# Optimization experiments

Hardware: AMD Instinct MI355X
Metric: run time of the kernel (lower is better)

The kernel has to match this reference:

```python
import jax, jax.numpy as jnp
import numpy as np

B, N, H = 32768, 64, 256
OFF = N * (N - 1) // 2  # 2016


def _xavier(k, shape):
    fan_in, fan_out = shape
    lim = (6.0 / (fan_in + fan_out)) ** 0.5
    return jax.random.uniform(k, shape, jnp.float32, -lim, lim)


def setup_inputs() -> dict:
    key = jax.random.key(0)
    ks = jax.random.split(key, 8)
    return {
        "x": jax.random.normal(ks[0], (B, N), jnp.float32),
        "Wd1": _xavier(ks[1], (N, H)), "bd1": jnp.zeros((H,), jnp.float32),
        "Wd2": _xavier(ks[2], (H, H)), "bd2": jnp.zeros((H,), jnp.float32),
        "Wdo": _xavier(ks[3], (H, N)), "bdo": jnp.zeros((N,), jnp.float32),
        "Wo1": _xavier(ks[4], (N, H)), "bo1": jnp.zeros((H,), jnp.float32),
        "Wo2": _xavier(ks[5], (H, H)), "bo2": jnp.zeros((H,), jnp.float32),
        "Woo": _xavier(ks[6], (H, OFF)), "boo": jnp.zeros((OFF,), jnp.float32),
        "damp_min": 0.01 * jnp.ones((N,), jnp.float32),
    }


def reference(x, Wd1, bd1, Wd2, bd2, Wdo, bdo,
              Wo1, bo1, Wo2, bo2, Woo, boo, damp_min):
    x0 = x  # [B, N]
    # diag branch MLP (tanh hidden layers)
    h = jnp.tanh(x0 @ Wd1 + bd1)
    h = jnp.tanh(h @ Wd2 + bd2)
    d = h @ Wdo + bdo                       # [B, N]
    diag = (jax.nn.relu(d) + damp_min) * x0  # [B, N]
    # off-diag branch MLP
    g = jnp.tanh(x0 @ Wo1 + bo1)
    g = jnp.tanh(g @ Wo2 + bo2)
    off = g @ Woo + boo                     # [B, N(N-1)/2]
    # scatter into batched lower-triangular L (static index sets)
    rows, cols = np.tril_indices(N, k=-1)
    di = np.arange(N)
    L = jnp.zeros((x0.shape[0], N, N), x0.dtype)
    L = L.at[:, rows, cols].set(off)
    L = L.at[:, di, di].set(diag)
    # D_i = (L_i L_i^T) x0_i == L_i (L_i^T x0_i)
    v = jnp.einsum('bji,bj->bi', L, x0)     # L^T x0
    return jnp.einsum('bij,bj->bi', L, v)   # [B, N]
```

## Files before the change

### kernel.cpp

```cpp
#include <hip/hip_runtime.h>


#define BT 32
#define THREADS 1024

typedef short short8 __attribute__((ext_vector_type(8)));
typedef float floatx4 __attribute__((ext_vector_type(4)));
typedef float float2v __attribute__((ext_vector_type(2)));
typedef int   intx4  __attribute__((ext_vector_type(4)));

#define S_W    2032.0f
#define S_W2   1016.0f
#define S_WDO  812.8f
#define S_G    127.0f
#define INV_SG (1.0f / (2032.0f * 127.0f))
#define INV_23 (1.0f / (1016.0f * 127.0f))
#define INV_DO (1.0f / (812.8f * 127.0f))

#if __has_builtin(__builtin_amdgcn_mfma_i32_16x16x64_i8)
#define MFMA_I8(acc, a, b) (acc) = __builtin_amdgcn_mfma_i32_16x16x64_i8((a), (b), (acc), 0, 0, 0)
#define MFMA_I8_FENCE()
#else
#define MFMA_I8(acc, a, b) asm("v_mfma_i32_16x16x64_i8 %0, %1, %2, %0" : "+v"(acc) : "v"(a), "v"(b))
#define MFMA_I8_FENCE() do { __builtin_amdgcn_sched_barrier(0); \
    asm volatile("s_nop 7\n\ts_nop 7\n\ts_nop 7"); } while (0)
#endif

__device__ __forceinline__ ushort f2bf(float f) {
    uint u = __builtin_bit_cast(uint, f);
    u += 0x7FFFu + ((u >> 16) & 1u);
    return (ushort)(u >> 16);
}
__device__ __forceinline__ uint cpk(float lo, float hi) {
    uint r;
    asm("v_cvt_pk_bf16_f32 %0, %1, %2" : "=v"(r) : "v"(lo), "v"(hi));
    return r;
}
__device__ __forceinline__ void pk_fma(float2v& d, float2v a, float2v b) {
    asm("v_pk_fma_f32 %0, %1, %2, %0" : "+v"(d) : "v"(a), "v"(b));
}
__device__ __forceinline__ float bf2f(ushort h) {
    return __builtin_bit_cast(float, ((uint)h) << 16);
}
__device__ __forceinline__ float bflo(uint u) { return __builtin_bit_cast(float, u << 16); }
__device__ __forceinline__ float bfhi(uint u) { return __builtin_bit_cast(float, u & 0xFFFF0000u); }

__device__ __forceinline__ float fast_tanh(float x) {
    float y = __expf(2.f * x) + 1.f;
    float r;
    asm("v_rcp_f32 %0, %1" : "=v"(r) : "v"(y));
    return fmaf(-2.f, r, 1.f);
}
__device__ __forceinline__ uint q4i8(float g0, float g1, float g2, float g3) {
    uint b0 = __builtin_bit_cast(uint, fmaf(g0, S_G, 12582912.f));
    uint b1 = __builtin_bit_cast(uint, fmaf(g1, S_G, 12582912.f));
    uint b2 = __builtin_bit_cast(uint, fmaf(g2, S_G, 12582912.f));
    uint b3 = __builtin_bit_cast(uint, fmaf(g3, S_G, 12582912.f));
    return (b0 & 255u) | ((b1 & 255u) << 8) | ((b2 & 255u) << 16) | (b3 << 24);
}
__device__ __forceinline__ int s8idx(int k) {
    int a = k >> 3, r = k & 7;
    return 8 * (r ? (a + 1) * (4 * a + r - 1) : a * (4 * a + 3));
}
__device__ __forceinline__ int trik(int p) {
    int kr = (int)sqrtf(2.f * (float)p);
    if (kr < 1) kr = 1;
    if (kr > 63) kr = 63;
    while (kr < 63 && s8idx(kr + 1) <= p) kr++;
    while (kr > 1 && s8idx(kr) > p) kr--;
    return kr;
}

__global__ __launch_bounds__(256)
void pack_all4(const float* __restrict__ Wd1, const float* __restrict__ Wd2,
               const float* __restrict__ Wdo, const float* __restrict__ Wo1,
               const float* __restrict__ Wo2, const float* __restrict__ Woo,
               const float* __restrict__ boo,
               ushort* __restrict__ ws, unsigned char* __restrict__ wi8,
               float* __restrict__ boo_p8) {
    const int bid = blockIdx.x, tid = threadIdx.x;
    if (bid >= 736) {
        int p = (bid - 736) * 256 + tid;
        if (p < 2240) {
            int kr = trik(p);
            int jj = p - s8idx(kr);
            boo_p8[p] = (jj < kr) ? boo[kr * (kr - 1) / 2 + jj] : 0.f;
        }
        return;
    }
    if (bid >= 32) {
        const float* W; unsigned char* dst; int Ncols, ntile, segb, woo = 0;
        float scale;
        if (bid < 96)       { W = Wd2; dst = wi8;          Ncols = 256;  ntile = 16;  segb = bid - 32;  scale = S_W2; }
        else if (bid < 160) { W = Wo2; dst = wi8 + 65536;  Ncols = 256;  ntile = 16;  segb = bid - 96;  scale = S_W2; }
        else if (bid < 176) { W = Wdo; dst = wi8 + 131072; Ncols = 64;   ntile = 4;   segb = bid - 160; scale = S_WDO; }
        else                { W = Woo; dst = wi8 + 147456; Ncols = 2016; ntile = 140; segb = bid - 176; scale = S_W; woo = 1; }
        int kblk = segb / ntile, tile = segb % ntile;
        __shared__ int colmap8[16];
        __shared__ signed char tr8[64][20];
        if (tid < 16) {
            int c = tile * 16 + tid;
            if (woo) {
                int kr = trik(c);
                int jj = c - s8idx(kr);
                c = (jj < kr) ? kr * (kr - 1) / 2 + jj : -1;
            }
            colmap8[tid] = c;
        }
        __syncthreads();
        {
            int r = tid >> 2, c0 = (tid & 3) * 4;
            const float* row = W + (size_t)(kblk * 64 + r) * Ncols;
#pragma unroll
            for (int i = 0; i < 4; i++) {
                int cm = colmap8[c0 + i];
                float v = (cm >= 0) ? row[cm] : 0.f;
                tr8[r][c0 + i] = (signed char)(int)__builtin_rintf(v * scale);
            }
        }
        __syncthreads();
        {
            int l = tid >> 2, j0 = (tid & 3) * 4;
            int q = l >> 4, ni = l & 15;
            uint pk = 0;
#pragma unroll
            for (int i = 0; i < 4; i++) {
                int b = (int)tr8[q * 16 + j0 + i][ni];
                pk |= ((uint)b & 255u) << (8 * i);
            }
            *(uint*)(dst + (size_t)tile * 4096 + kblk * 1024 + tid * 4) = pk;
        }
        return;
    }
    const float* W; int base_us, segb;
    if (bid < 16) { W = Wd1; base_us = 0;     segb = bid; }
    else          { W = Wo1; base_us = 16384; segb = bid - 16; }
    const int tile = segb;

    __shared__ ushort tr[64][18];
    {
        int r = tid >> 2, c0 = (tid & 3) * 4;
        const float* row = W + (size_t)r * 256 + tile * 16;
#pragma unroll
        for (int i = 0; i < 4; i++)
            tr[r][c0 + i] = f2bf(row[c0 + i]);
    }
    __syncthreads();
    {
        int e = tid * 4;
        int ktl = e >> 9, rem = e & 511;
        int q = rem >> 7, j0 = rem & 7;
        int ni = (rem >> 3) & 15;
        ushort v0 = tr[ktl * 32 + q * 8 + j0 + 0][ni];
        ushort v1 = tr[ktl * 32 + q * 8 + j0 + 1][ni];
        ushort v2 = tr[ktl * 32 + q * 8 + j0 + 2][ni];
        ushort v3 = tr[ktl * 32 + q * 8 + j0 + 3][ni];
        uint2 o;
        o.x = (uint)v0 | ((uint)v1 << 16);
        o.y = (uint)v2 | ((uint)v3 << 16);
        *(uint2*)(ws + (size_t)base_us + (size_t)(tile * 2 + ktl) * 512 + rem) = o;
    }
}

#define BSTR8 2248
#define XBF_STR 88
#define A8STR 272
#define DGSTR 72
#define ACT_D8  8192
#define ACT_O8  16896
#define ACT_D28 25600
#define ACT_O28 34304
#define XS_B   143872
#define DG_B   152064
#define VB_B   156672
#define LDS_BYTES 161280

#define FRAGW(p, idx) (*(const short8*)((p) + (size_t)(idx) * 512 + (size_t)lane * 8))

#define LOADT(dst, t) do { \
    const intx4* fp_ = (const intx4*)(woo8 + (size_t)(t) * 4096 + (size_t)lane * 16); \
    _Pragma("unroll") \
    for (int kt_ = 0; kt_ < 4; kt_++) (dst)[kt_] = fp_[kt_ * 64]; \
} while (0)

#define COMPT(src, t) do { \
    intx4 alo_ = {0, 0, 0, 0}, ahi_ = {0, 0, 0, 0}; \
    _Pragma("unroll") \
    for (int kt_ = 0; kt_ < 4; kt_++) { \
        MFMA_I8(alo_, (src)[kt_], bfl8[kt_]); \
        MFMA_I8(ahi_, (src)[kt_], bfh8[kt_]); \
    } \
    MFMA_I8_FENCE(); \
    int p0_ = (t) * 16 + q * 4; \
    float4 bias_ = *(const float4*)(boo_p8 + p0_); \
    uint2 pw_; \
    pw_.x = cpk(fmaf((float)alo_[0], INV_SG, bias_.x), fmaf((float)alo_[1], INV_SG, bias_.y)); \
    pw_.y = cpk(fmaf((float)alo_[2], INV_SG, bias_.z), fmaf((float)alo_[3], INV_SG, bias_.w)); \
    *(uint2*)(off8 + ni * BSTR8 + p0_) = pw_; \
    pw_.x = cpk(fmaf((float)ahi_[0], INV_SG, bias_.x), fmaf((float)ahi_[1], INV_SG, bias_.y)); \
    pw_.y = cpk(fmaf((float)ahi_[2], INV_SG, bias_.z), fmaf((float)ahi_[3], INV_SG, bias_.w)); \
    *(uint2*)(off8 + (16 + ni) * BSTR8 + p0_) = pw_; \
} while (0)

__global__ __launch_bounds__(THREADS, 4)
void damping_fused(const float* __restrict__ x,
                   const ushort* __restrict__ wd1f, const ushort* __restrict__ wo1f,
                   const unsigned char* __restrict__ wd28,
                   const unsigned char* __restrict__ wo28,
                   const unsigned char* __restrict__ wdo8,
                   const unsigned char* __restrict__ woo8,
                   const float* __restrict__ bd1, const float* __restrict__ bd2,
                   const float* __restrict__ bdo, const float* __restrict__ bo1,
                   const float* __restrict__ bo2, const float* __restrict__ boo_p8,
                   const float* __restrict__ dmin, float* __restrict__ out) {
    extern __shared__ char smem[];
    ushort* off8   = (ushort*)smem;
    ushort* xbf    = (ushort*)smem;
    unsigned char* act_d8  = (unsigned char*)(smem + ACT_D8);
    unsigned char* act_o8  = (unsigned char*)(smem + ACT_O8);
    unsigned char* act_d28 = (unsigned char*)(smem + ACT_D28);
    unsigned char* act_o28 = (unsigned char*)(smem + ACT_O28);
    float*  xs     = (float*)(smem + XS_B);
    ushort* dgb    = (ushort*)(smem + DG_B);
    ushort* vb     = (ushort*)(smem + VB_B);

    const int tid  = threadIdx.x;
    const int lane = tid & 63;
    const int w    = tid >> 6;
    const int q    = lane >> 4;
    const int ni   = lane & 15;
    const int b0   = blockIdx.x * BT;

    if (tid < 512) {
        int row = tid >> 4;
        int c = (tid & 15) * 4;
        const float4 xv = *(const float4*)(x + (size_t)(b0 + row) * 64 + c);
        float* xr = xs + row * 64 + c;
        xr[0] = xv.x; xr[1] = xv.y; xr[2] = xv.z; xr[3] = xv.w;
        uint2 p;
        p.x = cpk(xv.x, xv.y);
        p.y = cpk(xv.z, xv.w);
        *(uint2*)(xbf + row * XBF_STR + c) = p;
    }
    __syncthreads();

    const int br = w >> 3;
    const int sp = w & 7;

    {
        const ushort* wf = br ? wo1f : wd1f;
        const float*  bs = br ? bo1 : bd1;
        unsigned char* aout = br ? act_o8 : act_d8;
        float4 bias[2];
        floatx4 acc[2][2];
#pragma unroll
        for (int tt = 0; tt < 2; tt++) {
            bias[tt] = *(const float4*)(bs + (sp * 2 + tt) * 16 + q * 4);
            acc[tt][0] = (floatx4){bias[tt].x, bias[tt].y, bias[tt].z, bias[tt].w};
            acc[tt][1] = acc[tt][0];
        }
        for (int kt = 0; kt < 2; kt++) {
            short8 bl = *(const short8*)(xbf + ni * XBF_STR + kt * 32 + q * 8);
            short8 bh = *(const short8*)(xbf + (16 + ni) * XBF_STR + kt * 32 + q * 8);
#pragma unroll
            for (int tt = 0; tt < 2; tt++) {
                short8 af = FRAGW(wf, (sp * 2 + tt) * 2 + kt);
                acc[tt][0] = __builtin_amdgcn_mfma_f32_16x16x32_bf16(af, bl, acc[tt][0], 0, 0, 0);
                acc[tt][1] = __builtin_amdgcn_mfma_f32_16x16x32_bf16(af, bh, acc[tt][1], 0, 0, 0);
            }
        }
#pragma unroll
        for (int tt = 0; tt < 2; tt++) {
            int col0 = (sp * 2 + tt) * 16 + q * 4;
#pragma unroll
            for (int hh = 0; hh < 2; hh++) {
                uint pk = q4i8(fast_tanh(acc[tt][hh][0]),
                               fast_tanh(acc[tt][hh][1]),
                               fast_tanh(acc[tt][hh][2]),
                               fast_tanh(acc[tt][hh][3]));
                *(uint*)(aout + (hh * 16 + ni) * A8STR + col0) = pk;
            }
        }
    }
    __syncthreads();

    {
        const unsigned char* wf8 = br ? wo28 : wd28;
        const float* bs = br ? bo2 : bd2;
        const unsigned char* ain = br ? act_o8 : act_d8;
        unsigned char* aout = br ? act_o28 : act_d28;
        intx4 acc[2][2] = {};
        for (int kt = 0; kt < 4; kt++) {
            intx4 bl = *(const intx4*)(ain + ni * A8STR + kt * 64 + q * 16);
            intx4 bh = *(const intx4*)(ain + (16 + ni) * A8STR + kt * 64 + q * 16);
#pragma unroll
            for (int tt = 0; tt < 2; tt++) {
                intx4 af = *(const intx4*)(wf8 + (size_t)(sp * 2 + tt) * 4096 + kt * 1024 + lane * 16);
                MFMA_I8(acc[tt][0], af, bl);
                MFMA_I8(acc[tt][1], af, bh);
            }
        }
        MFMA_I8_FENCE();
#pragma unroll
        for (int tt = 0; tt < 2; tt++) {
            int col0 = (sp * 2 + tt) * 16 + q * 4;
            float4 bias = *(const float4*)(bs + col0);
#pragma unroll
            for (int hh = 0; hh < 2; hh++) {
                uint pk = q4i8(fast_tanh(fmaf((float)acc[tt][hh][0], INV_23, bias.x)),
                               fast_tanh(fmaf((float)acc[tt][hh][1], INV_23, bias.y)),
                               fast_tanh(fmaf((float)acc[tt][hh][2], INV_23, bias.z)),
                               fast_tanh(fmaf((float)acc[tt][hh][3], INV_23, bias.w)));
                *(uint*)(aout + (hh * 16 + ni) * A8STR + col0) = pk;
            }
        }
    }
    __syncthreads();

    intx4 bfl8[4], bfh8[4];
#pragma unroll
    for (int kt = 0; kt < 4; kt++) {
        bfl8[kt] = *(const intx4*)(act_o28 + ni * A8STR + kt * 64 + q * 16);
        bfh8[kt] = *(const intx4*)(act_o28 + (16 + ni) * A8STR + kt * 64 + q * 16);
    }
    const int ts = (w + 12) & 15;
    const int nT = (ts < 12) ? 9 : 8;
    intx4 Af[4], Bf[4];
    LOADT(Af, ts);

    if (w < 4) {
        intx4 acc[2] = {};
        for (int kt = 0; kt < 4; kt++) {
            intx4 bl = *(const intx4*)(act_d28 + ni * A8STR + kt * 64 + q * 16);
            intx4 bh = *(const intx4*)(act_d28 + (16 + ni) * A8STR + kt * 64 + q * 16);
            intx4 af = *(const intx4*)(wdo8 + (size_t)w * 4096 + kt * 1024 + lane * 16);
            MFMA_I8(acc[0], af, bl);
            MFMA_I8(acc[1], af, bh);
        }
        MFMA_I8_FENCE();
        int col0 = w * 16 + q * 4;
        float4 bias = *(const float4*)(bdo + col0);
        float4 dmv  = *(const float4*)(dmin + col0);
#pragma unroll
        for (int hh = 0; hh < 2; hh++) {
            int rB = hh * 16 + ni;
            float d, g0, g1, g2, g3;
            d = fmaf((float)acc[hh][0], INV_DO, bias.x); g0 = ((d > 0.f) ? d : 0.f) + dmv.x;
            d = fmaf((float)acc[hh][1], INV_DO, bias.y); g1 = ((d > 0.f) ? d : 0.f) + dmv.y;
            d = fmaf((float)acc[hh][2], INV_DO, bias.z); g2 = ((d > 0.f) ? d : 0.f) + dmv.z;
            d = fmaf((float)acc[hh][3], INV_DO, bias.w); g3 = ((d > 0.f) ? d : 0.f) + dmv.w;
            g0 *= xs[rB * 64 + col0];
            g1 *= xs[rB * 64 + col0 + 1];
            g2 *= xs[rB * 64 + col0 + 2];
            g3 *= xs[rB * 64 + col0 + 3];
            uint2 p;
            p.x = cpk(g0, g1);
            p.y = cpk(g2, g3);
            *(uint2*)(dgb + rB * DGSTR + col0) = p;
        }
    }
    __syncthreads();

    {
        int tp = ts, it = 0;
        while (true) {
            bool more = (it + 1 < nT);
            if (more) LOADT(Bf, tp + 16);
            COMPT(Af, tp);
            ++it; tp += 16;
            if (!more) break;
            more = (it + 1 < nT);
            if (more) LOADT(Af, tp + 16);
            COMPT(Bf, tp);
            ++it; tp += 16;
            if (!more) break;
        }
    }
    __syncthreads();

    const int ko = lane >> 3, jb = lane & 7;
    int toff[8];
#pragma unroll
    for (int kk = 0; kk < 8; kk++) toff[kk] = s8idx(kk * 8 + ko) + 8 * jb;
    const int bA = w * 2, bB = bA + 1;
    const ushort* rowA = off8 + bA * BSTR8;
    const ushort* rowB = rowA + BSTR8;

    {
        float2v sA0 = {0.f, 0.f}, sA1 = {0.f, 0.f}, sA2 = {0.f, 0.f}, sA3 = {0.f, 0.f};
        float2v sB0 = {0.f, 0.f}, sB1 = {0.f, 0.f}, sB2 = {0.f, 0.f}, sB3 = {0.f, 0.f};
#pragma unroll
        for (int kk = 0; kk < 8; kk++) {
            int k = kk * 8 + ko;
            uint4 uA = *(const uint4*)(rowA + toff[kk]);
            uint4 uB = *(const uint4*)(rowB + toff[kk]);
            float xkA = xs[bA * 64 + k];
            float xkB = xs[bB * 64 + k];
            bool live = (8 * jb < k);
            xkA = live ? xkA : 0.f;
            xkB = live ? xkB : 0.f;
            float2v xA2 = {xkA, xkA}, xB2 = {xkB, xkB};
            float2v p;
            p = (float2v){bflo(uA.x), bfhi(uA.x)}; pk_fma(sA0, p, xA2);
            p = (float2v){bflo(uB.x), bfhi(uB.x)}; pk_fma(sB0, p, xB2);
            p = (float2v){bflo(uA.y), bfhi(uA.y)}; pk_fma(sA1, p, xA2);
            p = (float2v){bflo(uB.y), bfhi(uB.y)}; pk_fma(sB1, p, xB2);
            p = (float2v){bflo(uA.z), bfhi(uA.z)}; pk_fma(sA2, p, xA2);
            p = (float2v){bflo(uB.z), bfhi(uB.z)}; pk_fma(sB2, p, xB2);
            p = (float2v){bflo(uA.w), bfhi(uA.w)}; pk_fma(sA3, p, xA2);
            p = (float2v){bflo(uB.w), bfhi(uB.w)}; pk_fma(sB3, p, xB2);
        }
        float s[16] = {sA0.x, sA0.y, sA1.x, sA1.y, sA2.x, sA2.y, sA3.x, sA3.y,
                       sB0.x, sB0.y, sB1.x, sB1.y, sB2.x, sB2.y, sB3.x, sB3.y};
#pragma unroll
        for (int e = 0; e < 16; e++) {
            s[e] += __shfl_xor(s[e], 8);
            s[e] += __shfl_xor(s[e], 16);
            s[e] += __shfl_xor(s[e], 32);
        }
        if (lane < 8) {
            int j0 = lane * 8;
#pragma unroll
            for (int r = 0; r < 2; r++) {
                int b = bA + r;
                float* sr = s + r * 8;
                uint4 d = *(const uint4*)(dgb + b * DGSTR + j0);
                float4 xa = *(const float4*)(xs + b * 64 + j0);
                float4 xc = *(const float4*)(xs + b * 64 + j0 + 4);
                sr[0] += bflo(d.x) * xa.x; sr[1] += bfhi(d.x) * xa.y;
                sr[2] += bflo(d.y) * xa.z; sr[3] += bfhi(d.y) * xa.w;
                sr[4] += bflo(d.z) * xc.x; sr[5] += bfhi(d.z) * xc.y;
                sr[6] += bflo(d.w) * xc.z; sr[7] += bfhi(d.w) * xc.w;
                uint4 o;
                o.x = cpk(sr[0], sr[1]); o.y = cpk(sr[2], sr[3]);
                o.z = cpk(sr[4], sr[5]); o.w = cpk(sr[6], sr[7]);
                *(uint4*)(vb + b * DGSTR + j0) = o;
            }
        }
    }

    {
        const short8 z8 = {};
#pragma unroll
        for (int r = 0; r < 2; r++) {
            int b = bA + r;
            const ushort* rowt = off8 + b * BSTR8;
            const ushort* vrow = vb + b * DGSTR;
            short8 bv0 = *(const short8*)(vrow + q * 8);
            short8 bv1 = *(const short8*)(vrow + 32 + q * 8);
            bv0 = (ni == 0) ? bv0 : z8;
            bv1 = (ni == 0) ? bv1 : z8;
#pragma unroll
            for (int ib = 0; ib < 4; ib++) {
                const int i0 = ib * 16;
                const int soff = s8idx(i0 + ni);
                floatx4 acc = {};
                {
                    short8 a = *(const short8*)(rowt + soff + q * 8);
                    if (ib < 2) a = (q * 8 < i0 + ni) ? a : z8;
                    acc = __builtin_amdgcn_mfma_f32_16x16x32_bf16(a, bv0, acc, 0, 0, 0);
                }
                if (ib >= 2) {
                    short8 a = *(const short8*)(rowt + soff + 32 + q * 8);
                    a = (32 + q * 8 < i0 + ni) ? a : z8;
                    acc = __builtin_amdgcn_mfma_f32_16x16x32_bf16(a, bv1, acc, 0, 0, 0);
                }
                if (ni == 0) {
                    int i = i0 + q * 4;
                    uint2 d  = *(const uint2*)(dgb + b * DGSTR + i);
                    uint2 vv = *(const uint2*)(vb + b * DGSTR + i);
                    float4 o;
                    o.x = fmaf(bflo(d.x), bflo(vv.x), acc[0]);
                    o.y = fmaf(bfhi(d.x), bfhi(vv.x), acc[1]);
                    o.z = fmaf(bflo(d.y), bflo(vv.y), acc[2]);
                    o.w = fmaf(bfhi(d.y), bfhi(vv.y), acc[3]);
                    *(float4*)(out + (size_t)(b0 + b) * 64 + i) = o;
                }
            }
        }
    }
}

extern "C" void kernel_launch(void* const* d_in, const int* in_sizes, int n_in,
                              void* d_out, int out_size, void* d_ws, size_t ws_size,
                              hipStream_t stream) {
    const float* x    = (const float*)d_in[0];
    const float* Wd1  = (const float*)d_in[1];
    const float* bd1  = (const float*)d_in[2];
    const float* Wd2  = (const float*)d_in[3];
    const float* bd2  = (const float*)d_in[4];
    const float* Wdo  = (const float*)d_in[5];
    const float* bdo  = (const float*)d_in[6];
    const float* Wo1  = (const float*)d_in[7];
    const float* bo1  = (const float*)d_in[8];
    const float* Wo2  = (const float*)d_in[9];
    const float* bo2  = (const float*)d_in[10];
    const float* Woo  = (const float*)d_in[11];
    const float* boo  = (const float*)d_in[12];
    const float* dmin = (const float*)d_in[13];
    float* out = (float*)d_out;

    ushort* ws   = (ushort*)d_ws;
    ushort* wd1f = ws;
    ushort* wo1f = ws + 16384;
    unsigned char* wi8  = (unsigned char*)d_ws + 65536;
    unsigned char* wd28 = wi8;
    unsigned char* wo28 = wi8 + 65536;
    unsigned char* wdo8 = wi8 + 131072;
    unsigned char* woo8 = wi8 + 147456;
    float*  boo_p8 = (float*)((unsigned char*)d_ws + 1507328);

    pack_all4<<<745, 256, 0, stream>>>(Wd1, Wd2, Wdo, Wo1, Wo2, Woo, boo,
                                       ws, wi8, boo_p8);

    hipFuncSetAttribute((const void*)damping_fused,
                        hipFuncAttributeMaxDynamicSharedMemorySize, LDS_BYTES);

    damping_fused<<<32768 / BT, THREADS, LDS_BYTES, stream>>>(
        x, wd1f, wo1f, wd28, wo28, wdo8, woo8,
        bd1, bd2, bdo, bo1, bo2, boo_p8, dmin, out);
}
```

Before: 158.2 us.

## Fuse weight packing into main kernel via cooperative launch with persistent rounds

```diff
diff --git a/kernel.cpp b/kernel.cpp
--- a/kernel.cpp
+++ b/kernel.cpp
@@ -1,8 +1,12 @@
 #include <hip/hip_runtime.h>
+#include <hip/hip_cooperative_groups.h>
+
+namespace cg = cooperative_groups;
 
 
 #define BT 32
 #define THREADS 1024
+#define NWG 256
 
 typedef short short8 __attribute__((ext_vector_type(8)));
 typedef float floatx4 __attribute__((ext_vector_type(4)));
@@ -69,97 +73,6 @@
     while (kr < 63 && s8idx(kr + 1) <= p) kr++;
     while (kr > 1 && s8idx(kr) > p) kr--;
     return kr;
-}
-
-__global__ __launch_bounds__(256)
-void pack_all4(const float* __restrict__ Wd1, const float* __restrict__ Wd2,
-               const float* __restrict__ Wdo, const float* __restrict__ Wo1,
-               const float* __restrict__ Wo2, const float* __restrict__ Woo,
-               const float* __restrict__ boo,
-               ushort* __restrict__ ws, unsigned char* __restrict__ wi8,
-               float* __restrict__ boo_p8) {
-    const int bid = blockIdx.x, tid = threadIdx.x;
-    if (bid >= 736) {
-        int p = (bid - 736) * 256 + tid;
-        if (p < 2240) {
-            int kr = trik(p);
-            int jj = p - s8idx(kr);
-            boo_p8[p] = (jj < kr) ? boo[kr * (kr - 1) / 2 + jj] : 0.f;
-        }
-        return;
-    }
-    if (bid >= 32) {
-        const float* W; unsigned char* dst; int Ncols, ntile, segb, woo = 0;
-        float scale;
-        if (bid < 96)       { W = Wd2; dst = wi8;          Ncols = 256;  ntile = 16;  segb = bid - 32;  scale = S_W2; }
-        else if (bid < 160) { W = Wo2; dst = wi8 + 65536;  Ncols = 256;  ntile = 16;  segb = bid - 96;  scale = S_W2; }
-        else if (bid < 176) { W = Wdo; dst = wi8 + 131072; Ncols = 64;   ntile = 4;   segb = bid - 160; scale = S_WDO; }
-        else                { W = Woo; dst = wi8 + 147456; Ncols = 2016; ntile = 140; segb = bid - 176; scale = S_W; woo = 1; }
-        int kblk = segb / ntile, tile = segb % ntile;
-        __shared__ int colmap8[16];
-        __shared__ signed char tr8[64][20];
-        if (tid < 16) {
-            int c = tile * 16 + tid;
-            if (woo) {
-                int kr = trik(c);
-                int jj = c - s8idx(kr);
-                c = (jj < kr) ? kr * (kr - 1) / 2 + jj : -1;
-            }
-            colmap8[tid] = c;
-        }
-        __syncthreads();
-        {
-            int r = tid >> 2, c0 = (tid & 3) * 4;
-            const float* row = W + (size_t)(kblk * 64 + r) * Ncols;
-#pragma unroll
-            for (int i = 0; i < 4; i++) {
-                int cm = colmap8[c0 + i];
-                float v = (cm >= 0) ? row[cm] : 0.f;
-                tr8[r][c0 + i] = (signed char)(int)__builtin_rintf(v * scale);
-            }
-        }
-        __syncthreads();
-        {
-            int l = tid >> 2, j0 = (tid & 3) * 4;
-            int q = l >> 4, ni = l & 15;
-            uint pk = 0;
-#pragma unroll
-            for (int i = 0; i < 4; i++) {
-                int b = (int)tr8[q * 16 + j0 + i][ni];
-                pk |= ((uint)b & 255u) << (8 * i);
-            }
-            *(uint*)(dst + (size_t)tile * 4096 + kblk * 1024 + tid * 4) = pk;
-        }
-        return;
-    }
-    const float* W; int base_us, segb;
-    if (bid < 16) { W = Wd1; base_us = 0;     segb = bid; }
-    else          { W = Wo1; base_us = 16384; segb = bid - 16; }
-    const int tile = segb;
-
-    __shared__ ushort tr[64][18];
-    {
-        int r = tid >> 2, c0 = (tid & 3) * 4;
-        const float* row = W + (size_t)r * 256 + tile * 16;
-#pragma unroll
-        for (int i = 0; i < 4; i++)
-            tr[r][c0 + i] = f2bf(row[c0 + i]);
-    }
-    __syncthreads();
-    {
-        int e = tid * 4;
-        int ktl = e >> 9, rem = e & 511;
-        int q = rem >> 7, j0 = rem & 7;
-        int ni = (rem >> 3) & 15;
-        ushort v0 = tr[ktl * 32 + q * 8 + j0 + 0][ni];
-        ushort v1 = tr[ktl * 32 + q * 8 + j0 + 1][ni];
-        ushort v2 = tr[ktl * 32 + q * 8 + j0 + 2][ni];
-        ushort v3 = tr[ktl * 32 + q * 8 + j0 + 3][ni];
-        uint2 o;
-        o.x = (uint)v0 | ((uint)v1 << 16);
-        o.y = (uint)v2 | ((uint)v3 << 16);
-        *(uint2*)(ws + (size_t)base_us + (size_t)(tile * 2 + ktl) * 512 + rem) = o;
-    }
 }
 
 #define BSTR8 2248
@@ -203,16 +116,17 @@
 } while (0)
 
 __global__ __launch_bounds__(THREADS, 4)
-void damping_fused(const float* __restrict__ x,
-                   const ushort* __restrict__ wd1f, const ushort* __restrict__ wo1f,
-                   const unsigned char* __restrict__ wd28,
-                   const unsigned char* __restrict__ wo28,
-                   const unsigned char* __restrict__ wdo8,
-                   const unsigned char* __restrict__ woo8,
-                   const float* __restrict__ bd1, const float* __restrict__ bd2,
-                   const float* __restrict__ bdo, const float* __restrict__ bo1,
-                   const float* __restrict__ bo2, const float* __restrict__ boo_p8,
-                   const float* __restrict__ dmin, float* __restrict__ out) {
+void damping_all(const float* __restrict__ x,
+                 const float* __restrict__ Wd1, const float* __restrict__ Wd2,
+                 const float* __restrict__ Wdo, const float* __restrict__ Wo1,
+                 const float* __restrict__ Wo2, const float* __restrict__ Woo,
+                 const float* __restrict__ boo,
+                 ushort* __restrict__ wd1f, ushort* __restrict__ wo1f,
+                 unsigned char* __restrict__ wi8, float* __restrict__ boo_p8,
+                 const float* __restrict__ bd1, const float* __restrict__ bd2,
+                 const float* __restrict__ bdo, const float* __restrict__ bo1,
+                 const float* __restrict__ bo2,
+                 const float* __restrict__ dmin, float* __restrict__ out) {
     extern __shared__ char smem[];
     ushort* off8   = (ushort*)smem;
     ushort* xbf    = (ushort*)smem;
@@ -223,261 +137,346 @@
     float*  xs     = (float*)(smem + XS_B);
     ushort* dgb    = (ushort*)(smem + DG_B);
     ushort* vb     = (ushort*)(smem + VB_B);
+    const unsigned char* wd28 = wi8;
+    const unsigned char* wo28 = wi8 + 65536;
+    const unsigned char* wdo8 = wi8 + 131072;
+    const unsigned char* woo8 = wi8 + 147456;
 
     const int tid  = threadIdx.x;
     const int lane = tid & 63;
     const int w    = tid >> 6;
     const int q    = lane >> 4;
     const int ni   = lane & 15;
-    const int b0   = blockIdx.x * BT;
-
-    if (tid < 512) {
-        int row = tid >> 4;
-        int c = (tid & 15) * 4;
-        const float4 xv = *(const float4*)(x + (size_t)(b0 + row) * 64 + c);
-        float* xr = xs + row * 64 + c;
-        xr[0] = xv.x; xr[1] = xv.y; xr[2] = xv.z; xr[3] = xv.w;
-        uint2 p;
-        p.x = cpk(xv.x, xv.y);
-        p.y = cpk(xv.z, xv.w);
-        *(uint2*)(xbf + row * XBF_STR + c) = p;
+
+    {
+        const int sb = tid >> 8, t2 = tid & 255;
+        const int bid = blockIdx.x * 4 + sb;
+        ushort* tr = (ushort*)smem + (size_t)sb * 1152;
+        signed char* tr8 = (signed char*)tr;
+
+        const float* W = nullptr; unsigned char* dst = nullptr;
+        int Ncols = 0, ntile = 0, segb = 0, woo = 0, i8p = 0, bf = 0;
+        float scale = 0.f;
+        int base_us = 0;
+        if (bid < 16)       { W = Wd1; base_us = 0;     bf = 1; }
+        else if (bid < 32)  { W = Wo1; base_us = 16384; bf = 1; }
+        else if (bid < 96)  { W = Wd2; dst = wi8;          Ncols = 256;  ntile = 16;  segb = bid - 32;  scale = S_W2;  i8p = 1; }
+        else if (bid < 160) { W = Wo2; dst = wi8 + 65536;  Ncols = 256;  ntile = 16;  segb = bid - 96;  scale = S_W2;  i8p = 1; }
+        else if (bid < 176) { W = Wdo; dst = wi8 + 131072; Ncols = 64;   ntile = 4;   segb = bid - 160; scale = S_WDO; i8p = 1; }
+        else if (bid < 736) { W = Woo; dst = wi8 + 147456; Ncols = 2016; ntile = 140; segb = bid - 176; scale = S_W;   i8p = 1; woo = 1; }
+        const int kblk = i8p ? segb / ntile : 0;
+        const int tile = i8p ? segb % ntile : (bf ? (bid & 15) : 0);
+
+        if (bid >= 736 && bid < 745) {
+            int p = (bid - 736) * 256 + t2;
+            if (p < 2240) {
+                int kr = trik(p);
+                int jj = p - s8idx(kr);
+                boo_p8[p] = (jj < kr) ? boo[kr * (kr - 1) / 2 + jj] : 0.f;
+            }
+        } else if (i8p) {
+            int r = t2 >> 2, c0q = (t2 & 3) * 4;
+            const float* row = W + (size_t)(kblk * 64 + r) * Ncols;
+#pragma unroll
+            for (int i = 0; i < 4; i++) {
+                int c = tile * 16 + c0q + i;
+                float v;
+                if (woo) {
+                    int kr = trik(c);
+                    int jj = c - s8idx(kr);
+                    v = (jj < kr) ? row[kr * (kr - 1) / 2 + jj] : 0.f;
+                } else {
+                    v = row[c];
+                }
+                tr8[r * 20 + c0q + i] = (signed char)(int)__builtin_rintf(v * scale);
+            }
+        } else if (bf) {
+            int r = t2 >> 2, c0q = (t2 & 3) * 4;
+            const float* row = W + (size_t)r * 256 + tile * 16;
+#pragma unroll
+            for (int i = 0; i < 4; i++)
+                tr[r * 18 + c0q + i] = f2bf(row[c0q + i]);
+        }
+        __syncthreads();
+        if (i8p) {
+            int l = t2 >> 2, j0 = (t2 & 3) * 4;
+            int qq = l >> 4, nn = l & 15;
+            uint pk = 0;
+#pragma unroll
+            for (int i = 0; i < 4; i++) {
+                int bb = (int)tr8[(qq * 16 + j0 + i) * 20 + nn];
+                pk |= ((uint)bb & 255u) << (8 * i);
+            }
+            *(uint*)(dst + (size_t)tile * 4096 + kblk * 1024 + t2 * 4) = pk;
+        } else if (bf) {
+            ushort* wsb = (bid < 16) ? wd1f : wo1f;
+            int e = t2 * 4;
+            int ktl = e >> 9, rem = e & 511;
+            int qq = rem >> 7, j0 = rem & 7;
+            int nn = (rem >> 3) & 15;
+            ushort v0 = tr[(ktl * 32 + qq * 8 + j0 + 0) * 18 + nn];
+            ushort v1 = tr[(ktl * 32 + qq * 8 + j0 + 1) * 18 + nn];
+            ushort v2 = tr[(ktl * 32 + qq * 8 + j0 + 2) * 18 + nn];
+            ushort v3 = tr[(ktl * 32 + qq * 8 + j0 + 3) * 18 + nn];
+            uint2 o;
+            o.x = (uint)v0 | ((uint)v1 << 16);
+            o.y = (uint)v2 | ((uint)v3 << 16);
+            *(uint2*)(wsb + (size_t)(tile * 2 + ktl) * 512 + rem) = o;
+        }
     }
-    __syncthreads();
+    cg::this_grid().sync();
 
     const int br = w >> 3;
     const int sp = w & 7;
-
-    {
-        const ushort* wf = br ? wo1f : wd1f;
-        const float*  bs = br ? bo1 : bd1;
-        unsigned char* aout = br ? act_o8 : act_d8;
-        float4 bias[2];
-        floatx4 acc[2][2];
-#pragma unroll
-        for (int tt = 0; tt < 2; tt++) {
-            bias[tt] = *(const float4*)(bs + (sp * 2 + tt) * 16 + q * 4);
-            acc[tt][0] = (floatx4){bias[tt].x, bias[tt].y, bias[tt].z, bias[tt].w};
-            acc[tt][1] = acc[tt][0];
-        }
-        for (int kt = 0; kt < 2; kt++) {
-            short8 bl = *(const short8*)(xbf + ni * XBF_STR + kt * 32 + q * 8);
-            short8 bh = *(const short8*)(xbf + (16 + ni) * XBF_STR + kt * 32 + q * 8);
-#pragma unroll
-            for (int tt = 0; tt < 2; tt++) {
-                short8 af = FRAGW(wf, (sp * 2 + tt) * 2 + kt);
-                acc[tt][0] = __builtin_amdgcn_mfma_f32_16x16x32_bf16(af, bl, acc[tt][0], 0, 0, 0);
-                acc[tt][1] = __builtin_amdgcn_mfma_f32_16x16x32_bf16(af, bh, acc[tt][1], 0, 0, 0);
-            }
-        }
-#pragma unroll
-        for (int tt = 0; tt < 2; tt++) {
-            int col0 = (sp * 2 + tt) * 16 + q * 4;
-#pragma unroll
-            for (int hh = 0; hh < 2; hh++) {
-                uint pk = q4i8(fast_tanh(acc[tt][hh][0]),
-                               fast_tanh(acc[tt][hh][1]),
-                               fast_tanh(acc[tt][hh][2]),
-                               fast_tanh(acc[tt][hh][3]));
-                *(uint*)(aout + (hh * 16 + ni) * A8STR + col0) = pk;
-            }
-        }
-    }
-    __syncthreads();
-
-    {
-        const unsigned char* wf8 = br ? wo28 : wd28;
-        const float* bs = br ? bo2 : bd2;
-        const unsigned char* ain = br ? act_o8 : act_d8;
-        unsigned char* aout = br ? act_o28 : act_d28;
-        intx4 acc[2][2] = {};
-        for (int kt = 0; kt < 4; kt++) {
-            intx4 bl = *(const intx4*)(ain + ni * A8STR + kt * 64 + q * 16);
-            intx4 bh = *(const intx4*)(ain + (16 + ni) * A8STR + kt * 64 + q * 16);
-#pragma unroll
-            for (int tt = 0; tt < 2; tt++) {
-                intx4 af = *(const intx4*)(wf8 + (size_t)(sp * 2 + tt) * 4096 + kt * 1024 + lane * 16);
-                MFMA_I8(acc[tt][0], af, bl);
-                MFMA_I8(acc[tt][1], af, bh);
-            }
-        }
-        MFMA_I8_FENCE();
-#pragma unroll
-        for (int tt = 0; tt < 2; tt++) {
-            int col0 = (sp * 2 + tt) * 16 + q * 4;
-            float4 bias = *(const float4*)(bs + col0);
-#pragma unroll
-            for (int hh = 0; hh < 2; hh++) {
-                uint pk = q4i8(fast_tanh(fmaf((float)acc[tt][hh][0], INV_23, bias.x)),
-                               fast_tanh(fmaf((float)acc[tt][hh][1], INV_23, bias.y)),
-                               fast_tanh(fmaf((float)acc[tt][hh][2], INV_23, bias.z)),
-                               fast_tanh(fmaf((float)acc[tt][hh][3], INV_23, bias.w)));
-                *(uint*)(aout + (hh * 16 + ni) * A8STR + col0) = pk;
-            }
-        }
-    }
-    __syncthreads();
-
-    intx4 bfl8[4], bfh8[4];
-#pragma unroll
-    for (int kt = 0; kt < 4; kt++) {
-        bfl8[kt] = *(const intx4*)(act_o28 + ni * A8STR + kt * 64 + q * 16);
-        bfh8[kt] = *(const intx4*)(act_o28 + (16 + ni) * A8STR + kt * 64 + q * 16);
-    }
     const int ts = (w + 12) & 15;
     const int nT = (ts < 12) ? 9 : 8;
-    intx4 Af[4], Bf[4];
-    LOADT(Af, ts);
-
-    if (w < 4) {
-        intx4 acc[2] = {};
+
+    for (int round = 0; round < 4; ++round) {
+        const int b0 = (blockIdx.x + round * NWG) * BT;
+
+        if (tid < 512) {
+            int row = tid >> 4;
+            int c = (tid & 15) * 4;
+            const float4 xv = *(const float4*)(x + (size_t)(b0 + row) * 64 + c);
+            float* xr = xs + row * 64 + c;
+            xr[0] = xv.x; xr[1] = xv.y; xr[2] = xv.z; xr[3] = xv.w;
+            uint2 p;
+            p.x = cpk(xv.x, xv.y);
+            p.y = cpk(xv.z, xv.w);
+            *(uint2*)(xbf + row * XBF_STR + c) = p;
+        }
+        __syncthreads();
+
+        {
+            const ushort* wf = br ? wo1f : wd1f;
+            const float*  bs = br ? bo1 : bd1;
+            unsigned char* aout = br ? act_o8 : act_d8;
+            float4 bias[2];
+            floatx4 acc[2][2];
+#pragma unroll
+            for (int tt = 0; tt < 2; tt++) {
+                bias[tt] = *(const float4*)(bs + (sp * 2 + tt) * 16 + q * 4);
+                acc[tt][0] = (floatx4){bias[tt].x, bias[tt].y, bias[tt].z, bias[tt].w};
+                acc[tt][1] = acc[tt][0];
+            }
+            for (int kt = 0; kt < 2; kt++) {
+                short8 bl = *(const short8*)(xbf + ni * XBF_STR + kt * 32 + q * 8);
+                short8 bh = *(const short8*)(xbf + (16 + ni) * XBF_STR + kt * 32 + q * 8);
+#pragma unroll
+                for (int tt = 0; tt < 2; tt++) {
+                    short8 af = FRAGW(wf, (sp * 2 + tt) * 2 + kt);
+                    acc[tt][0] = __builtin_amdgcn_mfma_f32_16x16x32_bf16(af, bl, acc[tt][0], 0, 0, 0);
+                    acc[tt][1] = __builtin_amdgcn_mfma_f32_16x16x32_bf16(af, bh, acc[tt][1], 0, 0, 0);
+                }
+            }
+#pragma unroll
+            for (int tt = 0; tt < 2; tt++) {
+                int col0 = (sp * 2 + tt) * 16 + q * 4;
+#pragma unroll
+                for (int hh = 0; hh < 2; hh++) {
+                    uint pk = q4i8(fast_tanh(acc[tt][hh][0]),
+                                   fast_tanh(acc[tt][hh][1]),
+                                   fast_tanh(acc[tt][hh][2]),
+                                   fast_tanh(acc[tt][hh][3]));
+                    *(uint*)(aout + (hh * 16 + ni) * A8STR + col0) = pk;
+                }
+            }
+        }
+        __syncthreads();
+
+        {
+            const unsigned char* wf8 = br ? wo28 : wd28;
+            const float* bs = br ? bo2 : bd2;
+            const unsigned char* ain = br ? act_o8 : act_d8;
+            unsigned char* aout = br ? act_o28 : act_d28;
+            intx4 acc[2][2] = {};
+            for (int kt = 0; kt < 4; kt++) {
+                intx4 bl = *(const intx4*)(ain + ni * A8STR + kt * 64 + q * 16);
+                intx4 bh = *(const intx4*)(ain + (16 + ni) * A8STR + kt * 64 + q * 16);
+#pragma unroll
+                for (int tt = 0; tt < 2; tt++) {
+                    intx4 af = *(const intx4*)(wf8 + (size_t)(sp * 2 + tt) * 4096 + kt * 1024 + lane * 16);
+                    MFMA_I8(acc[tt][0], af, bl);
+                    MFMA_I8(acc[tt][1], af, bh);
+                }
+            }
+            MFMA_I8_FENCE();
+#pragma unroll
+            for (int tt = 0; tt < 2; tt++) {
+                int col0 = (sp * 2 + tt) * 16 + q * 4;
+                float4 bias = *(const float4*)(bs + col0);
+#pragma unroll
+                for (int hh = 0; hh < 2; hh++) {
+                    uint pk = q4i8(fast_tanh(fmaf((float)acc[tt][hh][0], INV_23, bias.x)),
+                                   fast_tanh(fmaf((float)acc[tt][hh][1], INV_23, bias.y)),
+                                   fast_tanh(fmaf((float)acc[tt][hh][2], INV_23, bias.z)),
+                                   fast_tanh(fmaf((float)acc[tt][hh][3], INV_23, bias.w)));
+                    *(uint*)(aout + (hh * 16 + ni) * A8STR + col0) = pk;
+                }
+            }
+        }
+        __syncthreads();
+
+        intx4 bfl8[4], bfh8[4];
+#pragma unroll
         for (int kt = 0; kt < 4; kt++) {
-            intx4 bl = *(const intx4*)(act_d28 + ni * A8STR + kt * 64 + q * 16);
-            intx4 bh = *(const intx4*)(act_d28 + (16 + ni) * A8STR + kt * 64 + q * 16);
-            intx4 af = *(const intx4*)(wdo8 + (size_t)w * 4096 + kt * 1024 + lane * 16);
-            MFMA_I8(acc[0], af, bl);
-            MFMA_I8(acc[1], af, bh);
-        }
-        MFMA_I8_FENCE();
-        int col0 = w * 16 + q * 4;
-        float4 bias = *(const float4*)(bdo + col0);
-        float4 dmv  = *(const float4*)(dmin + col0);
-#pragma unroll
-        for (int hh = 0; hh < 2; hh++) {
-            int rB = hh * 16 + ni;
-            float d, g0, g1, g2, g3;
-            d = fmaf((float)acc[hh][0], INV_DO, bias.x); g0 = ((d > 0.f) ? d : 0.f) + dmv.x;
-            d = fmaf((float)acc[hh][1], INV_DO, bias.y); g1 = ((d > 0.f) ? d : 0.f) + dmv.y;
-            d = fmaf((float)acc[hh][2], INV_DO, bias.z); g2 = ((d > 0.f) ? d : 0.f) + dmv.z;
-            d = fmaf((float)acc[hh][3], INV_DO, bias.w); g3 = ((d > 0.f) ? d : 0.f) + dmv.w;
-            g0 *= xs[rB * 64 + col0];
-            g1 *= xs[rB * 64 + col0 + 1];
-            g2 *= xs[rB * 64 + col0 + 2];
-            g3 *= xs[rB * 64 + col0 + 3];
-            uint2 p;
-            p.x = cpk(g0, g1);
-            p.y = cpk(g2, g3);
-            *(uint2*)(dgb + rB * DGSTR + col0) = p;
-        }
-    }
-    __syncthreads();
-
-    {
-        int tp = ts, it = 0;
-        while (true) {
-            bool more = (it + 1 < nT);
-            if (more) LOADT(Bf, tp + 16);
-            COMPT(Af, tp);
-            ++it; tp += 16;
-            if (!more) break;
-            more = (it + 1 < nT);
-            if (more) LOADT(Af, tp + 16);
-            COMPT(Bf, tp);
-            ++it; tp += 16;
-            if (!more) break;
-        }
-    }
-    __syncthreads();
-
-    const int ko = lane >> 3, jb = lane & 7;
-    int toff[8];
-#pragma unroll
-    for (int kk = 0; kk < 8; kk++) toff[kk] = s8idx(kk * 8 + ko) + 8 * jb;
-    const int bA = w * 2, bB = bA + 1;
-    const ushort* rowA = off8 + bA * BSTR8;
-    const ushort* rowB = rowA + BSTR8;
-
-    {
-        float2v sA0 = {0.f, 0.f}, sA1 = {0.f, 0.f}, sA2 = {0.f, 0.f}, sA3 = {0.f, 0.f};
-        float2v sB0 = {0.f, 0.f}, sB1 = {0.f, 0.f}, sB2 = {0.f, 0.f}, sB3 = {0.f, 0.f};
-#pragma unroll
-        for (int kk = 0; kk < 8; kk++) {
-            int k = kk * 8 + ko;
-            uint4 uA = *(const uint4*)(rowA + toff[kk]);
-            uint4 uB = *(const uint4*)(rowB + toff[kk]);
-            float xkA = xs[bA * 64 + k];
-            float xkB = xs[bB * 64 + k];
-            bool live = (8 * jb < k);
-            xkA = live ? xkA : 0.f;
-            xkB = live ? xkB : 0.f;
-            float2v xA2 = {xkA, xkA}, xB2 = {xkB, xkB};
-            float2v p;
-            p = (float2v){bflo(uA.x), bfhi(uA.x)}; pk_fma(sA0, p, xA2);
-            p = (float2v){bflo(uB.x), bfhi(uB.x)}; pk_fma(sB0, p, xB2);
-            p = (float2v){bflo(uA.y), bfhi(uA.y)}; pk_fma(sA1, p, xA2);
-            p = (float2v){bflo(uB.y), bfhi(uB.y)}; pk_fma(sB1, p, xB2);
-            p = (float2v){bflo(uA.z), bfhi(uA.z)}; pk_fma(sA2, p, xA2);
-            p = (float2v){bflo(uB.z), bfhi(uB.z)}; pk_fma(sB2, p, xB2);
-            p = (float2v){bflo(uA.w), bfhi(uA.w)}; pk_fma(sA3, p, xA2);
-            p = (float2v){bflo(uB.w), bfhi(uB.w)}; pk_fma(sB3, p, xB2);
-        }
-        float s[16] = {sA0.x, sA0.y, sA1.x, sA1.y, sA2.x, sA2.y, sA3.x, sA3.y,
-                       sB0.x, sB0.y, sB1.x, sB1.y, sB2.x, sB2.y, sB3.x, sB3.y};
-#pragma unroll
-        for (int e = 0; e < 16; e++) {
-            s[e] += __shfl_xor(s[e], 8);
-            s[e] += __shfl_xor(s[e], 16);
-            s[e] += __shfl_xor(s[e], 32);
-        }
-        if (lane < 8) {
-            int j0 = lane * 8;
+            bfl8[kt] = *(const intx4*)(act_o28 + ni * A8STR + kt * 64 + q * 16);
+            bfh8[kt] = *(const intx4*)(act_o28 + (16 + ni) * A8STR + kt * 64 + q * 16);
+        }
+        intx4 Af[4], Bf[4];
+        LOADT(Af, ts);
+
+        if (w < 4) {
+            intx4 acc[2] = {};
+            for (int kt = 0; kt < 4; kt++) {
+                intx4 bl = *(const intx4*)(act_d28 + ni * A8STR + kt * 64 + q * 16);
+                intx4 bh = *(const intx4*)(act_d28 + (16 + ni) * A8STR + kt * 64 + q * 16);
+                intx4 af = *(const intx4*)(wdo8 + (size_t)w * 4096 + kt * 1024 + lane * 16);
+                MFMA_I8(acc[0], af, bl);
+                MFMA_I8(acc[1], af, bh);
+            }
+            MFMA_I8_FENCE();
+            int col0 = w * 16 + q * 4;
+            float4 bias = *(const float4*)(bdo + col0);
+            float4 dmv  = *(const float4*)(dmin + col0);
+#pragma unroll
+            for (int hh = 0; hh < 2; hh++) {
+                int rB = hh * 16 + ni;
+                float d, g0, g1, g2, g3;
+                d = fmaf((float)acc[hh][0], INV_DO, bias.x); g0 = ((d > 0.f) ? d : 0.f) + dmv.x;
+                d = fmaf((float)acc[hh][1], INV_DO, bias.y); g1 = ((d > 0.f) ? d : 0.f) + dmv.y;
+                d = fmaf((float)acc[hh][2], INV_DO, bias.z); g2 = ((d > 0.f) ? d : 0.f) + dmv.z;
+                d = fmaf((float)acc[hh][3], INV_DO, bias.w); g3 = ((d > 0.f) ? d : 0.f) + dmv.w;
+                g0 *= xs[rB * 64 + col0];
+                g1 *= xs[rB * 64 + col0 + 1];
+                g2 *= xs[rB * 64 + col0 + 2];
+                g3 *= xs[rB * 64 + col0 + 3];
+                uint2 p;
+                p.x = cpk(g0, g1);
+                p.y = cpk(g2, g3);
+                *(uint2*)(dgb + rB * DGSTR + col0) = p;
+            }
+        }
+        __syncthreads();
+
+        {
+            int tp = ts, it = 0;
+            while (true) {
+                bool more = (it + 1 < nT);
+                if (more) LOADT(Bf, tp + 16);
+                COMPT(Af, tp);
+                ++it; tp += 16;
+                if (!more) break;
+                more = (it + 1 < nT);
+                if (more) LOADT(Af, tp + 16);
+                COMPT(Bf, tp);
+                ++it; tp += 16;
+                if (!more) break;
+            }
+        }
+        __syncthreads();
+
+        const int ko = lane >> 3, jb = lane & 7;
+        int toff[8];
+#pragma unroll
+        for (int kk = 0; kk < 8; kk++) toff[kk] = s8idx(kk * 8 + ko) + 8 * jb;
+        const int bA = w * 2, bB = bA + 1;
+        const ushort* rowA = off8 + bA * BSTR8;
+        const ushort* rowB = rowA + BSTR8;
+        {
+            float2v sA0 = {0.f, 0.f}, sA1 = {0.f, 0.f}, sA2 = {0.f, 0.f}, sA3 = {0.f, 0.f};
+            float2v sB0 = {0.f, 0.f}, sB1 = {0.f, 0.f}, sB2 = {0.f, 0.f}, sB3 = {0.f, 0.f};
+#pragma unroll
+            for (int kk = 0; kk < 8; kk++) {
+                int k = kk * 8 + ko;
+                uint4 uA = *(const uint4*)(rowA + toff[kk]);
+                uint4 uB = *(const uint4*)(rowB + toff[kk]);
+                float xkA = xs[bA * 64 + k];
+                float xkB = xs[bB * 64 + k];
+                bool live = (8 * jb < k);
+                xkA = live ? xkA : 0.f;
+                xkB = live ? xkB : 0.f;
+                float2v xA2 = {xkA, xkA}, xB2 = {xkB, xkB};
+                float2v p;
+                p = (float2v){bflo(uA.x), bfhi(uA.x)}; pk_fma(sA0, p, xA2);
+                p = (float2v){bflo(uB.x), bfhi(uB.x)}; pk_fma(sB0, p, xB2);
+                p = (float2v){bflo(uA.y), bfhi(uA.y)}; pk_fma(sA1, p, xA2);
+                p = (float2v){bflo(uB.y), bfhi(uB.y)}; pk_fma(sB1, p, xB2);
+                p = (float2v){bflo(uA.z), bfhi(uA.z)}; pk_fma(sA2, p, xA2);
+                p = (float2v){bflo(uB.z), bfhi(uB.z)}; pk_fma(sB2, p, xB2);
+                p = (float2v){bflo(uA.w), bfhi(uA.w)}; pk_fma(sA3, p, xA2);
+                p = (float2v){bflo(uB.w), bfhi(uB.w)}; pk_fma(sB3, p, xB2);
+            }
+            float s[16] = {sA0.x, sA0.y, sA1.x, sA1.y, sA2.x, sA2.y, sA3.x, sA3.y,
+                           sB0.x, sB0.y, sB1.x, sB1.y, sB2.x, sB2.y, sB3.x, sB3.y};
+#pragma unroll
+            for (int e = 0; e < 16; e++) {
+                s[e] += __shfl_xor(s[e], 8);
+                s[e] += __shfl_xor(s[e], 16);
+                s[e] += __shfl_xor(s[e], 32);
+            }
+            if (lane < 8) {
+                int j0 = lane * 8;
+#pragma unroll
+                for (int r = 0; r < 2; r++) {
+                    int b = bA + r;
+                    float* sr = s + r * 8;
+                    uint4 d = *(const uint4*)(dgb + b * DGSTR + j0);
+                    float4 xa = *(const float4*)(xs + b * 64 + j0);
+                    float4 xc = *(const float4*)(xs + b * 64 + j0 + 4);
+                    sr[0] += bflo(d.x) * xa.x; sr[1] += bfhi(d.x) * xa.y;
+                    sr[2] += bflo(d.y) * xa.z; sr[3] += bfhi(d.y) * xa.w;
+                    sr[4] += bflo(d.z) * xc.x; sr[5] += bfhi(d.z) * xc.y;
+                    sr[6] += bflo(d.w) * xc.z; sr[7] += bfhi(d.w) * xc.w;
+                    uint4 o;
+                    o.x = cpk(sr[0], sr[1]); o.y = cpk(sr[2], sr[3]);
+                    o.z = cpk(sr[4], sr[5]); o.w = cpk(sr[6], sr[7]);
+                    *(uint4*)(vb + b * DGSTR + j0) = o;
+                }
+            }
+        }
+
+        {
+            const short8 z8 = {};
 #pragma unroll
             for (int r = 0; r < 2; r++) {
                 int b = bA + r;
-                float* sr = s + r * 8;
-                uint4 d = *(const uint4*)(dgb + b * DGSTR + j0);
-                float4 xa = *(const float4*)(xs + b * 64 + j0);
-                float4 xc = *(const float4*)(xs + b * 64 + j0 + 4);
-                sr[0] += bflo(d.x) * xa.x; sr[1] += bfhi(d.x) * xa.y;
-                sr[2] += bflo(d.y) * xa.z; sr[3] += bfhi(d.y) * xa.w;
-                sr[4] += bflo(d.z) * xc.x; sr[5] += bfhi(d.z) * xc.y;
-                sr[6] += bflo(d.w) * xc.z; sr[7] += bfhi(d.w) * xc.w;
-                uint4 o;
-                o.x = cpk(sr[0], sr[1]); o.y = cpk(sr[2], sr[3]);
-                o.z = cpk(sr[4], sr[5]); o.w = cpk(sr[6], sr[7]);
-                *(uint4*)(vb + b * DGSTR + j0) = o;
-            }
-        }
-    }
-
-    {
-        const short8 z8 = {};
-#pragma unroll
-        for (int r = 0; r < 2; r++) {
-            int b = bA + r;
-            const ushort* rowt = off8 + b * BSTR8;
-            const ushort* vrow = vb + b * DGSTR;
-            short8 bv0 = *(const short8*)(vrow + q * 8);
-            short8 bv1 = *(const short8*)(vrow + 32 + q * 8);
-            bv0 = (ni == 0) ? bv0 : z8;
-            bv1 = (ni == 0) ? bv1 : z8;
-#pragma unroll
-            for (int ib = 0; ib < 4; ib++) {
-                const int i0 = ib * 16;
-                const int soff = s8idx(i0 + ni);
-                floatx4 acc = {};
-                {
-                    short8 a = *(const short8*)(rowt + soff + q * 8);
-                    if (ib < 2) a = (q * 8 < i0 + ni) ? a : z8;
-                    acc = __builtin_amdgcn_mfma_f32_16x16x32_bf16(a, bv0, acc, 0, 0, 0);
-                }
-                if (ib >= 2) {
-                    short8 a = *(const short8*)(rowt + soff + 32 + q * 8);
-                    a = (32 + q * 8 < i0 + ni) ? a : z8;
-                    acc = __builtin_amdgcn_mfma_f32_16x16x32_bf16(a, bv1, acc, 0, 0, 0);
-                }
-                if (ni == 0) {
-                    int i = i0 + q * 4;
-                    uint2 d  = *(const uint2*)(dgb + b * DGSTR + i);
-                    uint2 vv = *(const uint2*)(vb + b * DGSTR + i);
-                    float4 o;
-                    o.x = fmaf(bflo(d.x), bflo(vv.x), acc[0]);
-                    o.y = fmaf(bfhi(d.x), bfhi(vv.x), acc[1]);
-                    o.z = fmaf(bflo(d.y), bflo(vv.y), acc[2]);
-                    o.w = fmaf(bfhi(d.y), bfhi(vv.y), acc[3]);
-                    *(float4*)(out + (size_t)(b0 + b) * 64 + i) = o;
-                }
-            }
-        }
+                const ushort* rowt = off8 + b * BSTR8;
+                const ushort* vrow = vb + b * DGSTR;
+                short8 bv0 = *(const short8*)(vrow + q * 8);
+                short8 bv1 = *(const short8*)(vrow + 32 + q * 8);
+                bv0 = (ni == 0) ? bv0 : z8;
+                bv1 = (ni == 0) ? bv1 : z8;
+#pragma unroll
+                for (int ib = 0; ib < 4; ib++) {
+                    const int i0 = ib * 16;
+                    const int soff = s8idx(i0 + ni);
+                    floatx4 acc = {};
+                    {
+                        short8 a = *(const short8*)(rowt + soff + q * 8);
+                        if (ib < 2) a = (q * 8 < i0 + ni) ? a : z8;
+                        acc = __builtin_amdgcn_mfma_f32_16x16x32_bf16(a, bv0, acc, 0, 0, 0);
+                    }
+                    if (ib >= 2) {
+                        short8 a = *(const short8*)(rowt + soff + 32 + q * 8);
+                        a = (32 + q * 8 < i0 + ni) ? a : z8;
+                        acc = __builtin_amdgcn_mfma_f32_16x16x32_bf16(a, bv1, acc, 0, 0, 0);
+                    }
+                    if (ni == 0) {
+                        int i = i0 + q * 4;
+                        uint2 d  = *(const uint2*)(dgb + b * DGSTR + i);
+                        uint2 vv = *(const uint2*)(vb + b * DGSTR + i);
+                        float4 o;
+                        o.x = fmaf(bflo(d.x), bflo(vv.x), acc[0]);
+                        o.y = fmaf(bfhi(d.x), bfhi(vv.x), acc[1]);
+                        o.z = fmaf(bflo(d.y), bflo(vv.y), acc[2]);
+                        o.w = fmaf(bfhi(d.y), bfhi(vv.y), acc[3]);
+                        *(float4*)(out + (size_t)(b0 + b) * 64 + i) = o;
+                    }
+                }
+            }
+        }
+        __syncthreads();
     }
 }
 
@@ -500,23 +499,21 @@
     const float* dmin = (const float*)d_in[13];
     float* out = (float*)d_out;
 
-    ushort* ws   = (ushort*)d_ws;
-    ushort* wd1f = ws;
-    ushort* wo1f = ws + 16384;
-    unsigned char* wi8  = (unsigned char*)d_ws + 65536;
-    unsigned char* wd28 = wi8;
-    unsigned char* wo28 = wi8 + 65536;
-    unsigned char* wdo8 = wi8 + 131072;
-    unsigned char* woo8 = wi8 + 147456;
-    float*  boo_p8 = (float*)((unsigned char*)d_ws + 1507328);
-
-    pack_all4<<<745, 256, 0, stream>>>(Wd1, Wd2, Wdo, Wo1, Wo2, Woo, boo,
-                                       ws, wi8, boo_p8);
-
-    hipFuncSetAttribute((const void*)damping_fused,
+    ushort* wd1f = (ushort*)d_ws;
+    ushort* wo1f = (ushort*)d_ws + 16384;
+    unsigned char* wi8 = (unsigned char*)d_ws + 65536;
+    float* boo_p8 = (float*)((unsigned char*)d_ws + 1507328);
+
+    hipFuncSetAttribute((const void*)damping_all,
                         hipFuncAttributeMaxDynamicSharedMemorySize, LDS_BYTES);
 
-    damping_fused<<<32768 / BT, THREADS, LDS_BYTES, stream>>>(
-        x, wd1f, wo1f, wd28, wo28, wdo8, woo8,
-        bd1, bd2, bdo, bo1, bo2, boo_p8, dmin, out);
-}
+    void* args[] = {
+        (void*)&x, (void*)&Wd1, (void*)&Wd2, (void*)&Wdo, (void*)&Wo1,
+        (void*)&Wo2, (void*)&Woo, (void*)&boo,
+        (void*)&wd1f, (void*)&wo1f, (void*)&wi8, (void*)&boo_p8,
+        (void*)&bd1, (void*)&bd2, (void*)&bdo, (void*)&bo1, (void*)&bo2,
+        (void*)&dmin, (void*)&out
+    };
+    hipLaunchCooperativeKernel((void*)damping_all, dim3(NWG), dim3(THREADS),
+                               args, LDS_BYTES, stream);
+}
```

New measurement: 240.3 us. +51.9%, slower.
